# Optimization experiments

Hardware: AMD Instinct MI355X
Metric: run time of the kernel (lower is better)

## Reference

```python
import jax, jax.numpy as jnp
import numpy as np

ALPHA = 5.0   # ATan surrogate sharpness
THETA = 1.0   # firing threshold
EPS = 1e-5    # BatchNorm eps

@jax.custom_vjp
def spike(x):
    # forward: heaviside; backward: ATan surrogate
    return (x >= 0.0).astype(x.dtype)

def _spike_fwd(x):
    return spike(x), x

def _spike_bwd(x, g):
    return (g * (ALPHA / 2.0) / (1.0 + (jnp.pi / 2.0 * ALPHA * x) ** 2),)

spike.defvjp(_spike_fwd, _spike_bwd)

def lif_layer(x, W, beta_p, gamma, bias, U0):
    # x: [B,T,J], W: [I,J] -> h: [B,T,I]
    h = jnp.einsum('btj,ij->bti', x, W)
    # BatchNorm1d in training mode: per-channel stats over B*T (biased var)
    mu = h.mean(axis=(0, 1))
    var = h.var(axis=(0, 1))
    h = (h - mu) * jax.lax.rsqrt(var + EPS) * gamma + bias
    beta = jax.nn.sigmoid(beta_p)  # [I]
    S0 = jnp.zeros_like(U0)

    def step(carry, xt):
        Ut, St = carry
        Ut = beta * (Ut - THETA * St) + (1.0 - beta) * xt  # soft reset
        St = spike(Ut - THETA)
        return (Ut, St), St

    _, o = jax.lax.scan(step, (U0, S0), jnp.swapaxes(h, 0, 1))  # [T,B,I]
    return jnp.swapaxes(o, 0, 1)  # [B,T,I]

def setup_inputs() -> dict:
    key = jax.random.key(0)
    B, T, J, H = 32, 1024, 1024, 2048
    ks = jax.random.split(key, 16)
    f32 = jnp.float32
    inp = {
        'x': jax.random.normal(ks[0], (B, T, J), f32),
        'W1': jax.random.normal(ks[1], (H, J), f32) / np.sqrt(J),
        'beta1': jax.random.uniform(ks[2], (H,), f32, 0.0, 4.0),
        'gamma1': jnp.ones((H,), f32),
        'bias1': jnp.zeros((H,), f32),
        'U01': jax.random.uniform(ks[3], (B, H), f32),
        'W2': jax.random.normal(ks[4], (H, H), f32) / np.sqrt(H),
        'beta2': jax.random.uniform(ks[5], (H,), f32, 0.0, 4.0),
        'gamma2': jnp.ones((H,), f32),
        'bias2': jnp.zeros((H,), f32),
        'U02': jax.random.uniform(ks[6], (B, H), f32),
        'W3': jax.random.normal(ks[7], (J, H), f32) / np.sqrt(H),
        'beta3': jax.random.uniform(ks[8], (J,), f32, 0.0, 4.0),
        'gamma3': jnp.ones((J,), f32),
        'bias3': jnp.zeros((J,), f32),
        'U03': jax.random.uniform(ks[9], (B, J), f32),
    }
    return inp

def reference(x, W1, beta1, gamma1, bias1, U01,
              W2, beta2, gamma2, bias2, U02,
              W3, beta3, gamma3, bias3, U03):
    h = lif_layer(x, W1, beta1, gamma1, bias1, U01)
    h = lif_layer(h, W2, beta2, gamma2, bias2, U02)
    h = lif_layer(h, W3, beta3, gamma3, bias3, U03)
    return h
```

## Files before the change

kernel.cpp:

```cpp
#include <hip/hip_runtime.h>
#include <hip/hip_bf16.h>
#include <cmath>

#define BB 32
#define TT 1024
#define JJ 1024
#define HH 2048
#define MM (BB * TT)
#define MHALF (MM / 2)

typedef short s8v __attribute__((ext_vector_type(8)));
typedef float f4v __attribute__((ext_vector_type(4)));
typedef unsigned int u4v __attribute__((ext_vector_type(4)));
union ABu { u4v u; s8v v; };

__device__ inline void split_bf16x3(float w, unsigned short& h,
                                    unsigned short& m, unsigned short& l) {
    __hip_bfloat16 bh = __float2bfloat16(w);
    const float fh = __bfloat162float(bh);
    const float r1 = w - fh;
    __hip_bfloat16 bm = __float2bfloat16(r1);
    const float fm = __bfloat162float(bm);
    __hip_bfloat16 bl = __float2bfloat16(r1 - fm);
    h = *(unsigned short*)&bh; m = *(unsigned short*)&bm; l = *(unsigned short*)&bl;
}

__global__ void split_w(const float* __restrict__ W,
                        unsigned short* __restrict__ ph,
                        unsigned short* __restrict__ pm,
                        unsigned short* __restrict__ pl, int n)
{
    const int i = blockIdx.x * 256 + threadIdx.x;
    if (i >= n) return;
    split_bf16x3(W[i], ph[i], pm[i], pl[i]);
}

__global__ __launch_bounds__(512) void mfma_spk_gemm(
    const unsigned long long* __restrict__ S,
    int Mstr,
    const unsigned short* __restrict__ Wh,
    const unsigned short* __restrict__ Wm,
    const unsigned short* __restrict__ Wl,
    float* __restrict__ CA,
    float* __restrict__ CB,
    float* __restrict__ part,
    int M, int N, int K)
{
    __shared__ __align__(16) unsigned short Blds[2][3][2][64][32];
    __shared__ float SredS[3][2][2][32];
    const int tid = threadIdx.x;
    const int wv = tid >> 6;
    const int lane = tid & 63;
    const int wm = wv >> 1, wn = wv & 1;
    const int r16 = lane & 15, quad = lane >> 4;
    const int bm = blockIdx.x * 512;
    const int bn = blockIdx.y * 64;
    const unsigned int q8 = quad * 8;

    f4v acc[8][2] = {};

    const int rl = lane >> 2, chl = lane & 3;
    const unsigned short* sW[3];
    size_t sOff[3];
    int sP[3], sKh[3], sQ[3];
#pragma unroll
    for (int i = 0; i < 3; ++i) {
        const int e = wv * 3 + i;
        const int p = e >> 3, kh = (e >> 2) & 1, q = e & 3;
        const int srow = q * 16 + rl;
        const int kc = (chl - (srow >> 1)) & 3;
        sW[i] = (p == 0) ? Wh : (p == 1) ? Wm : Wl;
        sOff[i] = (size_t)(bn + srow) * K + kh * 32 + kc * 8;
        sP[i] = p; sKh[i] = kh; sQ[i] = q;
    }

    size_t abase[8];
#pragma unroll
    for (int ms = 0; ms < 8; ++ms)
        abase[ms] = (size_t)(bm + wm * 128 + ms * 16 + r16);

    int bR[2], bC[2];
#pragma unroll
    for (int ns = 0; ns < 2; ++ns) {
        bR[ns] = wn * 32 + ns * 16 + r16;
        bC[ns] = ((quad + (bR[ns] >> 1)) & 3) * 8;
    }

    auto stageB = [&](int buf, int i, int k0) {
        __builtin_amdgcn_global_load_lds(
            (const __attribute__((address_space(1))) void*)(sW[i] + sOff[i] + k0),
            (__attribute__((address_space(3))) void*)&Blds[buf][sP[i]][sKh[i]][sQ[i] * 16][0],
            16, 0, 0);
    };

    const int NT = K >> 6;

    unsigned long long a64A[8], a64B[8];
#pragma unroll
    for (int ms = 0; ms < 8; ++ms) a64A[ms] = S[abase[ms]];
#pragma unroll
    for (int i = 0; i < 3; ++i) stageB(0, i, 0);
    __syncthreads();

#define SPK_STEP(CURA, NXTA, CURL, NXTL, T)                                  \
    do {                                                                     \
        if ((T) + 1 < NT) {                                                  \
            _Pragma("unroll")                                                \
            for (int i = 0; i < 3; ++i) stageB((NXTL), i, ((T) + 1) << 6);   \
            _Pragma("unroll")                                                \
            for (int ms = 0; ms < 8; ++ms)                                   \
                NXTA[ms] = S[(size_t)((T) + 1) * Mstr + abase[ms]];          \
        }                                                                    \
        s8v afr[2][8];                                                       \
        _Pragma("unroll")                                                    \
        for (int ms = 0; ms < 8; ++ms) {                                     \
            const unsigned int w0 = (unsigned int)CURA[ms];                  \
            const unsigned int w1 = (unsigned int)(CURA[ms] >> 32);          \
            _Pragma("unroll")                                                \
            for (int kh = 0; kh < 2; ++kh) {                                 \
                const unsigned int w = kh ? w1 : w0;                         \
                const unsigned int bl = (w >> q8) & 0xFu;                    \
                const unsigned int bh = (w >> (q8 + 4)) & 0xFu;              \
                const unsigned int lo = (bl * 0x00204081u) & 0x01010101u;    \
                const unsigned int hi = (bh * 0x00204081u) & 0x01010101u;    \
                ABu tu;                                                      \
                tu.u[0] = __builtin_amdgcn_perm(0u, lo, 0x04010400u) * 0x3F80u; \
                tu.u[1] = __builtin_amdgcn_perm(0u, lo, 0x04030402u) * 0x3F80u; \
                tu.u[2] = __builtin_amdgcn_perm(0u, hi, 0x04010400u) * 0x3F80u; \
                tu.u[3] = __builtin_amdgcn_perm(0u, hi, 0x04030402u) * 0x3F80u; \
                afr[kh][ms] = tu.v;                                          \
            }                                                                \
        }                                                                    \
        _Pragma("unroll")                                                    \
        for (int p = 0; p < 3; ++p)                                          \
            _Pragma("unroll")                                                \
            for (int kh = 0; kh < 2; ++kh) {                                 \
                s8v bf[2];                                                   \
                _Pragma("unroll")                                            \
                for (int ns = 0; ns < 2; ++ns)                               \
                    bf[ns] = *(const s8v*)&Blds[CURL][p][kh][bR[ns]][bC[ns]];\
                __builtin_amdgcn_s_setprio(1);                               \
                _Pragma("unroll")                                            \
                for (int ms = 0; ms < 8; ++ms)                               \
                    _Pragma("unroll")                                        \
                    for (int ns = 0; ns < 2; ++ns)                           \
                        acc[ms][ns] = __builtin_amdgcn_mfma_f32_16x16x32_bf16( \
                            afr[kh][ms], bf[ns], acc[ms][ns], 0, 0, 0);      \
                __builtin_amdgcn_s_setprio(0);                               \
            }                                                                \
        if ((T) + 1 < NT) __syncthreads();                                   \
    } while (0)

    for (int t = 0; t < NT; t += 2) {
        SPK_STEP(a64A, a64B, 0, 1, t);
        SPK_STEP(a64B, a64A, 1, 0, t + 1);
    }
#undef SPK_STEP

    float s1v[2], s2v[2];
#pragma unroll
    for (int ns = 0; ns < 2; ++ns) {
        float s = 0.f, s2 = 0.f;
#pragma unroll
        for (int ms = 0; ms < 8; ++ms)
#pragma unroll
            for (int r = 0; r < 4; ++r) {
                const float v = acc[ms][ns][r];
                s += v;
                s2 = fmaf(v, v, s2);
            }
        s += __shfl_down(s, 32);  s += __shfl_down(s, 16);
        s2 += __shfl_down(s2, 32); s2 += __shfl_down(s2, 16);
        s1v[ns] = s; s2v[ns] = s2;
    }
    __syncthreads();
    if (wm > 0 && lane < 16) {
#pragma unroll
        for (int ns = 0; ns < 2; ++ns) {
            SredS[wm - 1][wn][0][ns * 16 + lane] = s1v[ns];
            SredS[wm - 1][wn][1][ns * 16 + lane] = s2v[ns];
        }
    }
    __syncthreads();
    if (wm == 0 && lane < 16) {
#pragma unroll
        for (int ns = 0; ns < 2; ++ns) {
            const int col = bn + wn * 32 + ns * 16 + lane;
            const int li = ns * 16 + lane;
            const float s  = s1v[ns] + SredS[0][wn][0][li] + SredS[1][wn][0][li] + SredS[2][wn][0][li];
            const float s2 = s2v[ns] + SredS[0][wn][1][li] + SredS[1][wn][1][li] + SredS[2][wn][1][li];
            part[((size_t)blockIdx.x * 2 + 0) * N + col] = s;
            part[((size_t)blockIdx.x * 2 + 1) * N + col] = s2;
        }
    }

    float* __restrict__ CO = (bm < MHALF) ? CA : CB;
    const int rsub = (bm < MHALF) ? 0 : MHALF;
#pragma unroll
    for (int ms = 0; ms < 8; ++ms)
#pragma unroll
        for (int ns = 0; ns < 2; ++ns) {
            const int row = bm - rsub + wm * 128 + ms * 16 + quad * 4;
            const int col = bn + wn * 32 + ns * 16 + r16;
#pragma unroll
            for (int r = 0; r < 4; ++r)
                CO[(size_t)(row + r) * N + col] = acc[ms][ns][r];
        }
}

struct Sp3 { unsigned int o0, o1, o2; };

__device__ inline Sp3 split_pair(float x, float y)
{
    const unsigned int xb = __float_as_uint(x), yb = __float_as_uint(y);
    const unsigned int x0 = xb & 0xFFFF0000u,  y0 = yb & 0xFFFF0000u;
    const float xr1 = x - __uint_as_float(x0), yr1 = y - __uint_as_float(y0);
    const unsigned int x1b = __float_as_uint(xr1), y1b = __float_as_uint(yr1);
    const unsigned int x1 = x1b & 0xFFFF0000u, y1 = y1b & 0xFFFF0000u;
    const float xr2 = xr1 - __uint_as_float(x1), yr2 = yr1 - __uint_as_float(y1);
    Sp3 r;
    r.o0 = __builtin_amdgcn_perm(yb, xb, 0x07060302u);
    r.o1 = __builtin_amdgcn_perm(y1b, x1b, 0x07060302u);
    r.o2 = __builtin_amdgcn_perm(__float_as_uint(yr2), __float_as_uint(xr2), 0x07060302u);
    return r;
}

__global__ __launch_bounds__(256) void mfma_f32x3_gemm(
    const float* __restrict__ A,
    const unsigned short* __restrict__ Wh,
    const unsigned short* __restrict__ Wm,
    const unsigned short* __restrict__ Wl,
    float* __restrict__ CA,
    float* __restrict__ CB,
    float* __restrict__ part,
    int M, int N, int K)
{
    __shared__ __align__(16) unsigned short Blds[2][3][128][32];
    __shared__ float SredF[2][2][64];
    const int tid = threadIdx.x;
    const int wv = tid >> 6;
    const int lane = tid & 63;
    const int wm = wv >> 1, wn = wv & 1;
    const int r16 = lane & 15, quad = lane >> 4;

    const int lin = blockIdx.y * 16 + blockIdx.x;
    const int ppx = gridDim.y >> 3;
    const int xcd = lin & 7, li = lin >> 3;
    const int pm = xcd * ppx + (li >> 4);
    const int pn = li & 15;
    const int bm = pm * 128;
    const int bn = pn * 128;

    f4v acc[4][4] = {};

    const int rl = lane >> 2, chl = lane & 3;
    size_t soff[2];
    int ldsrow[2];
#pragma unroll
    for (int i = 0; i < 2; ++i) {
        const int r = i * 64 + wv * 16 + rl;
        const int kc = (chl - (r >> 1)) & 3;
        soff[i] = (size_t)(bn + r) * K + kc * 8;
        ldsrow[i] = i * 64 + wv * 16;
    }

    size_t aoff[4];
#pragma unroll
    for (int ms = 0; ms < 4; ++ms)
        aoff[ms] = (size_t)(bm + wm * 64 + ms * 16 + r16) * K + quad * 8;

    int bR[4], bC[4];
#pragma unroll
    for (int ns = 0; ns < 4; ++ns) {
        bR[ns] = wn * 64 + ns * 16 + r16;
        bC[ns] = ((quad + (bR[ns] >> 1)) & 3) * 8;
    }

    auto stage = [&](int buf, int p, int i, int k0) {
        const unsigned short* Wp = (p == 0) ? Wh : (p == 1) ? Wm : Wl;
        __builtin_amdgcn_global_load_lds(
            (const __attribute__((address_space(1))) void*)(Wp + soff[i] + k0),
            (__attribute__((address_space(3))) void*)&Blds[buf][p][ldsrow[i]][0], 16, 0, 0);
    };

    float4 av[4][2];
#pragma unroll
    for (int ms = 0; ms < 4; ++ms) {
        av[ms][0] = *(const float4*)(A + aoff[ms]);
        av[ms][1] = *(const float4*)(A + aoff[ms] + 4);
    }
#pragma unroll
    for (int p = 0; p < 3; ++p)
#pragma unroll
        for (int i = 0; i < 2; ++i) stage(0, p, i, 0);
    __syncthreads();

    const int NT = K >> 5;
    for (int t = 0; t < NT; ++t) {
        const int cur = t & 1, nxt = cur ^ 1;
        const int k0 = t << 5;

        if (t + 1 < NT) {
#pragma unroll
            for (int p = 0; p < 3; ++p)
#pragma unroll
                for (int i = 0; i < 2; ++i) stage(nxt, p, i, k0 + 32);
        }

        s8v afr[3][4];
#pragma unroll
        for (int ms = 0; ms < 4; ++ms) {
            ABu t0, t1, t2;
            const float4 v0 = av[ms][0];
            const float4 v1 = av[ms][1];
            const Sp3 s0 = split_pair(v0.x, v0.y);
            const Sp3 s1 = split_pair(v0.z, v0.w);
            const Sp3 s2 = split_pair(v1.x, v1.y);
            const Sp3 s3 = split_pair(v1.z, v1.w);
            t0.u[0] = s0.o0; t1.u[0] = s0.o1; t2.u[0] = s0.o2;
            t0.u[1] = s1.o0; t1.u[1] = s1.o1; t2.u[1] = s1.o2;
            t0.u[2] = s2.o0; t1.u[2] = s2.o1; t2.u[2] = s2.o2;
            t0.u[3] = s3.o0; t1.u[3] = s3.o1; t2.u[3] = s3.o2;
            afr[0][ms] = t0.v;
            afr[1][ms] = t1.v;
            afr[2][ms] = t2.v;
        }
        if (t + 1 < NT) {
#pragma unroll
            for (int ms = 0; ms < 4; ++ms) {
                av[ms][0] = *(const float4*)(A + aoff[ms] + k0 + 32);
                av[ms][1] = *(const float4*)(A + aoff[ms] + k0 + 32 + 4);
            }
        }

#pragma unroll
        for (int pw = 0; pw < 3; ++pw) {
            s8v bf[4];
#pragma unroll
            for (int ns = 0; ns < 4; ++ns)
                bf[ns] = *(const s8v*)&Blds[cur][pw][bR[ns]][bC[ns]];
            __builtin_amdgcn_s_setprio(1);
#pragma unroll
            for (int pa = 0; pa + pw < 3; ++pa)
#pragma unroll
                for (int ms = 0; ms < 4; ++ms)
#pragma unroll
                    for (int ns = 0; ns < 4; ++ns)
                        acc[ms][ns] = __builtin_amdgcn_mfma_f32_16x16x32_bf16(
                            afr[pa][ms], bf[ns], acc[ms][ns], 0, 0, 0);
            __builtin_amdgcn_s_setprio(0);
        }

        if (t + 1 < NT) __syncthreads();
    }

    float s1v[4], s2v[4];
#pragma unroll
    for (int ns = 0; ns < 4; ++ns) {
        float s = 0.f, s2 = 0.f;
#pragma unroll
        for (int ms = 0; ms < 4; ++ms)
#pragma unroll
            for (int r = 0; r < 4; ++r) {
                const float v = acc[ms][ns][r];
                s += v;
                s2 = fmaf(v, v, s2);
            }
        s += __shfl_down(s, 32);  s += __shfl_down(s, 16);
        s2 += __shfl_down(s2, 32); s2 += __shfl_down(s2, 16);
        s1v[ns] = s; s2v[ns] = s2;
    }
    __syncthreads();
    if (wm == 1 && lane < 16) {
#pragma unroll
        for (int ns = 0; ns < 4; ++ns) {
            SredF[wn][0][ns * 16 + lane] = s1v[ns];
            SredF[wn][1][ns * 16 + lane] = s2v[ns];
        }
    }
    __syncthreads();
    if (wm == 0 && lane < 16) {
#pragma unroll
        for (int ns = 0; ns < 4; ++ns) {
            const int col = bn + wn * 64 + ns * 16 + lane;
            const int li = ns * 16 + lane;
            part[((size_t)pm * 2 + 0) * N + col] = s1v[ns] + SredF[wn][0][li];
            part[((size_t)pm * 2 + 1) * N + col] = s2v[ns] + SredF[wn][1][li];
        }
    }

    float* __restrict__ CO = (bm < MHALF) ? CA : CB;
    const int rsub = (bm < MHALF) ? 0 : MHALF;
#pragma unroll
    for (int ms = 0; ms < 4; ++ms)
#pragma unroll
        for (int ns = 0; ns < 4; ++ns) {
            const int row = bm - rsub + wm * 64 + ms * 16 + quad * 4;
            const int col = bn + wn * 64 + ns * 16 + r16;
#pragma unroll
            for (int r = 0; r < 4; ++r)
                CO[(size_t)(row + r) * N + col] = acc[ms][ns][r];
        }
}

#define RCHUNK 128

__global__ void bn_stats_final(const float* __restrict__ partial,
                               float* __restrict__ stats,
                               int N, int nchunks)
{
    const int n = blockIdx.x * 256 + threadIdx.x;
    double s = 0.0, s2 = 0.0;
    for (int c = 0; c < nchunks; ++c) {
        s  += (double)partial[((size_t)c * 2 + 0) * N + n];
        s2 += (double)partial[((size_t)c * 2 + 1) * N + n];
    }
    const double inv_m = 1.0 / (double)MM;
    const double mu = s * inv_m;
    const double var = s2 * inv_m - mu * mu;
    stats[n]     = (float)mu;
    stats[N + n] = (float)(1.0 / sqrt(var + 1e-5));
}

#define LIF_STEP_PACK(hv)                                            \
    do {                                                             \
        const float hn = ((hv) - mu) * rstd * g + bi;                \
        u = beta * (u - s) + omb * hn;                               \
        const bool sp = (u - 1.0f) >= 0.f;                           \
        s = sp ? 1.f : 0.f;                                          \
        const unsigned long long mball = __ballot(sp);               \
        if (lead) bits[widx] = mball;                                \
        ++widx;                                                      \
    } while (0)

#define LIF_LOAD8(buf, tbase)                                        \
    _Pragma("unroll")                                                \
    for (int j = 0; j < 8; ++j) {                                    \
        const int tl = (tbase) + j;                                  \
        buf[j] = h[base + (size_t)(tl < TT ? tl : TT - 1) * N];      \
    }

__global__ __launch_bounds__(64) void bn_lif_scan_pack2(
    const float* __restrict__ hA,
    const float* __restrict__ hB,
    unsigned long long* __restrict__ bits,
    const float* __restrict__ stats,
    const float* __restrict__ gamma,
    const float* __restrict__ bias,
    const float* __restrict__ beta_p,
    const float* __restrict__ U0,
    int N)
{
    const int n = blockIdx.x * 64 + threadIdx.x;
    const int b = blockIdx.y;
    const float* __restrict__ h = (b < BB / 2) ? hA : hB;
    const int bl = b & (BB / 2 - 1);
    const float mu = stats[n];
    const float rstd = stats[N + n];
    const float g = gamma[n];
    const float bi = bias[n];
    const float beta = 1.f / (1.f + expf(-beta_p[n]));
    const float omb = 1.f - beta;
    float u = U0[(size_t)b * N + n];
    float s = 0.f;
    const size_t base = ((size_t)bl * TT) * N + n;
    size_t widx = (size_t)(n >> 6) * (size_t)MM + (size_t)b * TT;
    const bool lead = (threadIdx.x & 63) == 0;

    float b0[8], b1[8], b2[8], b3[8];
    LIF_LOAD8(b0, 0);
    LIF_LOAD8(b1, 8);
    LIF_LOAD8(b2, 16);
    for (int t0 = 0; t0 < TT; t0 += 32) {
        LIF_LOAD8(b3, t0 + 24);
#pragma unroll
        for (int j = 0; j < 8; ++j) { const float hv = b0[j]; LIF_STEP_PACK(hv); }
        LIF_LOAD8(b0, t0 + 32);
#pragma unroll
        for (int j = 0; j < 8; ++j) { const float hv = b1[j]; LIF_STEP_PACK(hv); }
        LIF_LOAD8(b1, t0 + 40);
#pragma unroll
        for (int j = 0; j < 8; ++j) { const float hv = b2[j]; LIF_STEP_PACK(hv); }
        LIF_LOAD8(b2, t0 + 48);
#pragma unroll
        for (int j = 0; j < 8; ++j) { const float hv = b3[j]; LIF_STEP_PACK(hv); }
    }
}

#define LIF_STEP_F32(hv)                                             \
    do {                                                             \
        const float hn = ((hv) - mu) * rstd * g + bi;                \
        u = beta * (u - s) + omb * hn;                               \
        s = ((u - 1.0f) >= 0.f) ? 1.f : 0.f;                         \
        out[oidx] = s;                                               \
        oidx += N;                                                   \
    } while (0)

__global__ __launch_bounds__(64) void bn_lif_scan_f32_2(
    const float* __restrict__ h,
    float* __restrict__ out,
    const float* __restrict__ stats,
    const float* __restrict__ gamma,
    const float* __restrict__ bias,
    const float* __restrict__ beta_p,
    const float* __restrict__ U0,
    int N)
{
    const int n = blockIdx.x * 64 + threadIdx.x;
    const int b = blockIdx.y;
    const float mu = stats[n];
    const float rstd = stats[N + n];
    const float g = gamma[n];
    const float bi = bias[n];
    const float beta = 1.f / (1.f + expf(-beta_p[n]));
    const float omb = 1.f - beta;
    float u = U0[(size_t)b * N + n];
    float s = 0.f;
    const size_t base = ((size_t)b * TT) * N + n;
    size_t oidx = base;

    float b0[8], b1[8], b2[8], b3[8];
    LIF_LOAD8(b0, 0);
    LIF_LOAD8(b1, 8);
    LIF_LOAD8(b2, 16);
    for (int t0 = 0; t0 < TT; t0 += 32) {
        LIF_LOAD8(b3, t0 + 24);
#pragma unroll
        for (int j = 0; j < 8; ++j) { const float hv = b0[j]; LIF_STEP_F32(hv); }
        LIF_LOAD8(b0, t0 + 32);
#pragma unroll
        for (int j = 0; j < 8; ++j) { const float hv = b1[j]; LIF_STEP_F32(hv); }
        LIF_LOAD8(b1, t0 + 40);
#pragma unroll
        for (int j = 0; j < 8; ++j) { const float hv = b2[j]; LIF_STEP_F32(hv); }
        LIF_LOAD8(b2, t0 + 48);
#pragma unroll
        for (int j = 0; j < 8; ++j) { const float hv = b3[j]; LIF_STEP_F32(hv); }
    }
}

extern "C" void kernel_launch(void* const* d_in, const int* in_sizes, int n_in,
                              void* d_out, int out_size, void* d_ws, size_t ws_size,
                              hipStream_t stream)
{
    const float* x   = (const float*)d_in[0];
    const float* W1  = (const float*)d_in[1];
    const float* bp1 = (const float*)d_in[2];
    const float* g1  = (const float*)d_in[3];
    const float* bi1 = (const float*)d_in[4];
    const float* U01 = (const float*)d_in[5];
    const float* W2  = (const float*)d_in[6];
    const float* bp2 = (const float*)d_in[7];
    const float* g2  = (const float*)d_in[8];
    const float* bi2 = (const float*)d_in[9];
    const float* U02 = (const float*)d_in[10];
    const float* W3  = (const float*)d_in[11];
    const float* bp3 = (const float*)d_in[12];
    const float* g3  = (const float*)d_in[13];
    const float* bi3 = (const float*)d_in[14];
    const float* U03 = (const float*)d_in[15];
    float* out = (float*)d_out;

    unsigned char* ws = (unsigned char*)d_ws;
    const size_t HA_BYTES  = (size_t)MHALF * HH * sizeof(float);
    const size_t SPK_BYTES = (size_t)MM * (HH / 8);
    float*              hA   = (float*)ws;
    float*              hB   = (float*)d_out;
    unsigned long long* spk  = (unsigned long long*)(ws + HA_BYTES);
    float*              part = (float*)(ws + HA_BYTES + SPK_BYTES);
    float*              stat = (float*)(ws + HA_BYTES + SPK_BYTES + 4194304);
    unsigned short*     W2h  = (unsigned short*)(ws + HA_BYTES + SPK_BYTES + 4194304 + 16384);
    unsigned short*     W2m  = W2h + (size_t)HH * HH;
    unsigned short*     W2l  = W2m + (size_t)HH * HH;
    unsigned short*     W3h  = W2l + (size_t)HH * HH;
    unsigned short*     W3m  = W3h + (size_t)JJ * HH;
    unsigned short*     W3l  = W3m + (size_t)JJ * HH;

    const dim3 blk(256);
    const dim3 blk64(64);
    const dim3 blk512(512);

    split_w<<<dim3((HH * JJ) / 256), blk, 0, stream>>>(W1, W2h, W2m, W2l, HH * JJ);
    mfma_f32x3_gemm<<<dim3(HH / 128, MM / 128), blk, 0, stream>>>(
        x, W2h, W2m, W2l, hA, hB, part, MM, HH, JJ);
    split_w<<<dim3((HH * HH) / 256), blk, 0, stream>>>(W2, W2h, W2m, W2l, HH * HH);
    split_w<<<dim3((JJ * HH) / 256), blk, 0, stream>>>(W3, W3h, W3m, W3l, JJ * HH);

    bn_stats_final<<<dim3(HH / 256), blk, 0, stream>>>(part, stat, HH, MM / 128);
    bn_lif_scan_pack2<<<dim3(HH / 64, BB), blk64, 0, stream>>>(
        hA, hB, spk, stat, g1, bi1, bp1, U01, HH);

    mfma_spk_gemm<<<dim3(MM / 512, HH / 64), blk512, 0, stream>>>(
        spk, MM, W2h, W2m, W2l, hA, hB, part, MM, HH, HH);
    bn_stats_final<<<dim3(HH / 256), blk, 0, stream>>>(part, stat, HH, MM / 512);
    bn_lif_scan_pack2<<<dim3(HH / 64, BB), blk64, 0, stream>>>(
        hA, hB, spk, stat, g2, bi2, bp2, U02, HH);

    mfma_spk_gemm<<<dim3(MM / 512, JJ / 64), blk512, 0, stream>>>(
        spk, MM, W3h, W3m, W3l, hA, hA + (size_t)MHALF * JJ, part, MM, JJ, HH);
    bn_stats_final<<<dim3(JJ / 256), blk, 0, stream>>>(part, stat, JJ, MM / 512);
    bn_lif_scan_f32_2<<<dim3(JJ / 64, BB), blk64, 0, stream>>>(
        hA, out, stat, g3, bi3, bp3, U03, JJ);
}
```

Measured before the change: 2.253 ms.

## Reshape spike GEMM tiles to 256x128 with K-step of 32

```diff
diff --git a/kernel.cpp b/kernel.cpp
--- a/kernel.cpp
+++ b/kernel.cpp
@@ -46,58 +46,60 @@
     float* __restrict__ part,
     int M, int N, int K)
 {
-    __shared__ __align__(16) unsigned short Blds[2][3][2][64][32];
-    __shared__ float SredS[3][2][2][32];
+    __shared__ __align__(16) unsigned short Blds[2][3][128][32];
+    __shared__ float SredS[3][2][2][64];
     const int tid = threadIdx.x;
     const int wv = tid >> 6;
     const int lane = tid & 63;
     const int wm = wv >> 1, wn = wv & 1;
     const int r16 = lane & 15, quad = lane >> 4;
-    const int bm = blockIdx.x * 512;
-    const int bn = blockIdx.y * 64;
+    const int bm = blockIdx.x * 256;
+    const int bn = blockIdx.y * 128;
     const unsigned int q8 = quad * 8;
 
-    f4v acc[8][2] = {};
+    f4v acc[4][4] = {};
 
     const int rl = lane >> 2, chl = lane & 3;
     const unsigned short* sW[3];
     size_t sOff[3];
-    int sP[3], sKh[3], sQ[3];
+    int sP[3], sR8[3];
 #pragma unroll
     for (int i = 0; i < 3; ++i) {
         const int e = wv * 3 + i;
-        const int p = e >> 3, kh = (e >> 2) & 1, q = e & 3;
-        const int srow = q * 16 + rl;
+        const int p = e >> 3, r8 = e & 7;
+        const int srow = r8 * 16 + rl;
         const int kc = (chl - (srow >> 1)) & 3;
         sW[i] = (p == 0) ? Wh : (p == 1) ? Wm : Wl;
-        sOff[i] = (size_t)(bn + srow) * K + kh * 32 + kc * 8;
-        sP[i] = p; sKh[i] = kh; sQ[i] = q;
-    }
-
-    size_t abase[8];
-#pragma unroll
-    for (int ms = 0; ms < 8; ++ms)
-        abase[ms] = (size_t)(bm + wm * 128 + ms * 16 + r16);
-
-    int bR[2], bC[2];
-#pragma unroll
-    for (int ns = 0; ns < 2; ++ns) {
-        bR[ns] = wn * 32 + ns * 16 + r16;
+        sOff[i] = (size_t)(bn + srow) * K + kc * 8;
+        sP[i] = p; sR8[i] = r8;
+    }
+
+    const unsigned int* __restrict__ S32 = (const unsigned int*)S;
+    const size_t MROW2 = 2 * (size_t)Mstr;
+    unsigned int abase2[4];
+#pragma unroll
+    for (int ms = 0; ms < 4; ++ms)
+        abase2[ms] = 2u * (unsigned)(bm + wm * 64 + ms * 16 + r16);
+
+    int bR[4], bC[4];
+#pragma unroll
+    for (int ns = 0; ns < 4; ++ns) {
+        bR[ns] = wn * 64 + ns * 16 + r16;
         bC[ns] = ((quad + (bR[ns] >> 1)) & 3) * 8;
     }
 
     auto stageB = [&](int buf, int i, int k0) {
         __builtin_amdgcn_global_load_lds(
             (const __attribute__((address_space(1))) void*)(sW[i] + sOff[i] + k0),
-            (__attribute__((address_space(3))) void*)&Blds[buf][sP[i]][sKh[i]][sQ[i] * 16][0],
+            (__attribute__((address_space(3))) void*)&Blds[buf][sP[i]][sR8[i] * 16][0],
             16, 0, 0);
     };
 
-    const int NT = K >> 6;
-
-    unsigned long long a64A[8], a64B[8];
-#pragma unroll
-    for (int ms = 0; ms < 8; ++ms) a64A[ms] = S[abase[ms]];
+    const int NT = K >> 5;
+
+    unsigned int a32A[4], a32B[4];
+#pragma unroll
+    for (int ms = 0; ms < 4; ++ms) a32A[ms] = S32[abase2[ms]];
 #pragma unroll
     for (int i = 0; i < 3; ++i) stageB(0, i, 0);
     __syncthreads();
@@ -106,63 +108,57 @@
     do {                                                                     \
         if ((T) + 1 < NT) {                                                  \
             _Pragma("unroll")                                                \
-            for (int i = 0; i < 3; ++i) stageB((NXTL), i, ((T) + 1) << 6);   \
+            for (int i = 0; i < 3; ++i) stageB((NXTL), i, ((T) + 1) << 5);   \
             _Pragma("unroll")                                                \
-            for (int ms = 0; ms < 8; ++ms)                                   \
-                NXTA[ms] = S[(size_t)((T) + 1) * Mstr + abase[ms]];          \
+            for (int ms = 0; ms < 4; ++ms)                                   \
+                NXTA[ms] = S32[(size_t)(((T) + 1) >> 1) * MROW2              \
+                               + abase2[ms] + (((T) + 1) & 1)];              \
         }                                                                    \
-        s8v afr[2][8];                                                       \
+        s8v afr[4];                                                          \
         _Pragma("unroll")                                                    \
-        for (int ms = 0; ms < 8; ++ms) {                                     \
-            const unsigned int w0 = (unsigned int)CURA[ms];                  \
-            const unsigned int w1 = (unsigned int)(CURA[ms] >> 32);          \
-            _Pragma("unroll")                                                \
-            for (int kh = 0; kh < 2; ++kh) {                                 \
-                const unsigned int w = kh ? w1 : w0;                         \
-                const unsigned int bl = (w >> q8) & 0xFu;                    \
-                const unsigned int bh = (w >> (q8 + 4)) & 0xFu;              \
-                const unsigned int lo = (bl * 0x00204081u) & 0x01010101u;    \
-                const unsigned int hi = (bh * 0x00204081u) & 0x01010101u;    \
-                ABu tu;                                                      \
-                tu.u[0] = __builtin_amdgcn_perm(0u, lo, 0x04010400u) * 0x3F80u; \
-                tu.u[1] = __builtin_amdgcn_perm(0u, lo, 0x04030402u) * 0x3F80u; \
-                tu.u[2] = __builtin_amdgcn_perm(0u, hi, 0x04010400u) * 0x3F80u; \
-                tu.u[3] = __builtin_amdgcn_perm(0u, hi, 0x04030402u) * 0x3F80u; \
-                afr[kh][ms] = tu.v;                                          \
-            }                                                                \
+        for (int ms = 0; ms < 4; ++ms) {                                     \
+            const unsigned int w = CURA[ms];                                 \
+            const unsigned int bl = (w >> q8) & 0xFu;                        \
+            const unsigned int bh = (w >> (q8 + 4)) & 0xFu;                  \
+            const unsigned int lo = (bl * 0x00204081u) & 0x01010101u;        \
+            const unsigned int hi = (bh * 0x00204081u) & 0x01010101u;        \
+            ABu tu;                                                          \
+            tu.u[0] = __builtin_amdgcn_perm(0u, lo, 0x04010400u) * 0x3F80u;  \
+            tu.u[1] = __builtin_amdgcn_perm(0u, lo, 0x04030402u) * 0x3F80u;  \
+            tu.u[2] = __builtin_amdgcn_perm(0u, hi, 0x04010400u) * 0x3F80u;  \
+            tu.u[3] = __builtin_amdgcn_perm(0u, hi, 0x04030402u) * 0x3F80u;  \
+            afr[ms] = tu.v;                                                  \
         }                                                                    \
         _Pragma("unroll")                                                    \
-        for (int p = 0; p < 3; ++p)                                          \
+        for (int p = 0; p < 3; ++p) {                                        \
+            s8v bf[4];                                                       \
             _Pragma("unroll")                                                \
-            for (int kh = 0; kh < 2; ++kh) {                                 \
-                s8v bf[2];                                                   \
+            for (int ns = 0; ns < 4; ++ns)                                   \
+                bf[ns] = *(const s8v*)&Blds[CURL][p][bR[ns]][bC[ns]];        \
+            __builtin_amdgcn_s_setprio(1);                                   \
+            _Pragma("unroll")                                                \
+            for (int ms = 0; ms < 4; ++ms)                                   \
                 _Pragma("unroll")                                            \
-                for (int ns = 0; ns < 2; ++ns)                               \
-                    bf[ns] = *(const s8v*)&Blds[CURL][p][kh][bR[ns]][bC[ns]];\
-                __builtin_amdgcn_s_setprio(1);                               \
-                _Pragma("unroll")                                            \
-                for (int ms = 0; ms < 8; ++ms)                               \
-                    _Pragma("unroll")                                        \
-                    for (int ns = 0; ns < 2; ++ns)                           \
-                        acc[ms][ns] = __builtin_amdgcn_mfma_f32_16x16x32_bf16( \
-                            afr[kh][ms], bf[ns], acc[ms][ns], 0, 0, 0);      \
-                __builtin_amdgcn_s_setprio(0);                               \
-            }                                                                \
+                for (int ns = 0; ns < 4; ++ns)                               \
+                    acc[ms][ns] = __builtin_amdgcn_mfma_f32_16x16x32_bf16(   \
+                        afr[ms], bf[ns], acc[ms][ns], 0, 0, 0);              \
+            __builtin_amdgcn_s_setprio(0);                                   \
+        }                                                                    \
         if ((T) + 1 < NT) __syncthreads();                                   \
     } while (0)
 
     for (int t = 0; t < NT; t += 2) {
-        SPK_STEP(a64A, a64B, 0, 1, t);
-        SPK_STEP(a64B, a64A, 1, 0, t + 1);
+        SPK_STEP(a32A, a32B, 0, 1, t);
+        SPK_STEP(a32B, a32A, 1, 0, t + 1);
     }
 #undef SPK_STEP
 
-    float s1v[2], s2v[2];
-#pragma unroll
-    for (int ns = 0; ns < 2; ++ns) {
+    float s1v[4], s2v[4];
+#pragma unroll
+    for (int ns = 0; ns < 4; ++ns) {
         float s = 0.f, s2 = 0.f;
 #pragma unroll
-        for (int ms = 0; ms < 8; ++ms)
+        for (int ms = 0; ms < 4; ++ms)
 #pragma unroll
             for (int r = 0; r < 4; ++r) {
                 const float v = acc[ms][ns][r];
@@ -176,7 +172,7 @@
     __syncthreads();
     if (wm > 0 && lane < 16) {
 #pragma unroll
-        for (int ns = 0; ns < 2; ++ns) {
+        for (int ns = 0; ns < 4; ++ns) {
             SredS[wm - 1][wn][0][ns * 16 + lane] = s1v[ns];
             SredS[wm - 1][wn][1][ns * 16 + lane] = s2v[ns];
         }
@@ -184,8 +180,8 @@
     __syncthreads();
     if (wm == 0 && lane < 16) {
 #pragma unroll
-        for (int ns = 0; ns < 2; ++ns) {
-            const int col = bn + wn * 32 + ns * 16 + lane;
+        for (int ns = 0; ns < 4; ++ns) {
+            const int col = bn + wn * 64 + ns * 16 + lane;
             const int li = ns * 16 + lane;
             const float s  = s1v[ns] + SredS[0][wn][0][li] + SredS[1][wn][0][li] + SredS[2][wn][0][li];
             const float s2 = s2v[ns] + SredS[0][wn][1][li] + SredS[1][wn][1][li] + SredS[2][wn][1][li];
@@ -197,11 +193,11 @@
     float* __restrict__ CO = (bm < MHALF) ? CA : CB;
     const int rsub = (bm < MHALF) ? 0 : MHALF;
 #pragma unroll
-    for (int ms = 0; ms < 8; ++ms)
-#pragma unroll
-        for (int ns = 0; ns < 2; ++ns) {
-            const int row = bm - rsub + wm * 128 + ms * 16 + quad * 4;
-            const int col = bn + wn * 32 + ns * 16 + r16;
+    for (int ms = 0; ms < 4; ++ms)
+#pragma unroll
+        for (int ns = 0; ns < 4; ++ns) {
+            const int row = bm - rsub + wm * 64 + ms * 16 + quad * 4;
+            const int col = bn + wn * 64 + ns * 16 + r16;
 #pragma unroll
             for (int r = 0; r < 4; ++r)
                 CO[(size_t)(row + r) * N + col] = acc[ms][ns][r];
@@ -402,8 +398,6 @@
                 CO[(size_t)(row + r) * N + col] = acc[ms][ns][r];
         }
 }
-
-#define RCHUNK 128
 
 __global__ void bn_stats_final(const float* __restrict__ partial,
                                float* __restrict__ stats,
@@ -590,15 +584,15 @@
     bn_lif_scan_pack2<<<dim3(HH / 64, BB), blk64, 0, stream>>>(
         hA, hB, spk, stat, g1, bi1, bp1, U01, HH);
 
-    mfma_spk_gemm<<<dim3(MM / 512, HH / 64), blk512, 0, stream>>>(
+    mfma_spk_gemm<<<dim3(MM / 256, HH / 128), blk512, 0, stream>>>(
         spk, MM, W2h, W2m, W2l, hA, hB, part, MM, HH, HH);
-    bn_stats_final<<<dim3(HH / 256), blk, 0, stream>>>(part, stat, HH, MM / 512);
+    bn_stats_final<<<dim3(HH / 256), blk, 0, stream>>>(part, stat, HH, MM / 256);
     bn_lif_scan_pack2<<<dim3(HH / 64, BB), blk64, 0, stream>>>(
         hA, hB, spk, stat, g2, bi2, bp2, U02, HH);
 
-    mfma_spk_gemm<<<dim3(MM / 512, JJ / 64), blk512, 0, stream>>>(
+    mfma_spk_gemm<<<dim3(MM / 256, JJ / 128), blk512, 0, stream>>>(
         spk, MM, W3h, W3m, W3l, hA, hA + (size_t)MHALF * JJ, part, MM, JJ, HH);
-    bn_stats_final<<<dim3(JJ / 256), blk, 0, stream>>>(part, stat, JJ, MM / 512);
+    bn_stats_final<<<dim3(JJ / 256), blk, 0, stream>>>(part, stat, JJ, MM / 256);
     bn_lif_scan_f32_2<<<dim3(JJ / 64, BB), blk64, 0, stream>>>(
         hA, out, stat, g3, bi3, bp3, U03, JJ);
 }
```

Measured after the change: 2.390 ms. 1.06x slower.
